# Kernel tuning notes

Measured on AMD Instinct MI355X. Metric: run time of the kernel, lower is better.

Reference implementation:

```python
import jax, jax.numpy as jnp
import numpy as np

C_CONST = 1.0
GAMMA = 1.0
GATE_EPS = 1e-9


def _gate(a, b):
    # smooth 'between' gate: ~1 when a*b < 0, ~0 when a*b > 0
    u = a * b
    return 0.5 * (1.0 - u / jnp.sqrt(u * u + GATE_EPS))


def _softmin2(a, b, gamma):
    return -gamma * jnp.logaddexp(-a / gamma, -b / gamma)


def _softmin3(a, b, c, gamma):
    s = jnp.stack([a, b, c], axis=0)
    return -gamma * jax.nn.logsumexp(-s / gamma, axis=0)


def _trans(x_val, y_prev, z_other, c, gamma):
    # MSM split/merge transition cost, soft version
    a = x_val - y_prev
    b = x_val - z_other
    g = _gate(a, b)
    return c + (1.0 - g) * _softmin2(a * a, b * b, gamma)


def _soft_msm_batched(xb, yb, c, gamma):
    # xb: (B, T), yb: (B, U) -> costs (B,)
    B, T = xb.shape
    U = yb.shape[1]
    # row 0: C[0,0] = (x0-y0)^2; C[0,j] = C[0,j-1] + trans(y_j, y_{j-1}, x_0)
    c00 = (xb[:, 0] - yb[:, 0]) ** 2                                  # (B,)
    left0 = _trans(yb[:, 1:], yb[:, :-1], xb[:, 0:1], c, gamma)       # (B, U-1)
    row0 = jnp.concatenate(
        [c00[:, None], c00[:, None] + jnp.cumsum(left0, axis=1)], axis=1
    )                                                                 # (B, U)

    def row_step(prev, xs):
        xi, xim1 = xs                                                 # (B,), (B,)
        match = (xi[:, None] - yb) ** 2                               # (B, U)
        up = _trans(xi[:, None], xim1[:, None], yb, c, gamma)         # (B, U)
        left = _trans(yb[:, 1:], yb[:, :-1], xi[:, None], c, gamma)   # (B, U-1)
        c_i0 = prev[:, 0] + up[:, 0]                                  # (B,)
        d_diag = prev[:, :-1] + match[:, 1:]                          # (B, U-1)
        d_up = prev[:, 1:] + up[:, 1:]                                # (B, U-1)

        def cell(c_left, z):
            dd, du, lf = z                                            # each (B,)
            cij = _softmin3(dd, du, c_left + lf, gamma)
            return cij, cij

        _, cells = jax.lax.scan(cell, c_i0, (d_diag.T, d_up.T, left.T))
        row = jnp.concatenate([c_i0[:, None], cells.T], axis=1)       # (B, U)
        return row, None

    last_row, _ = jax.lax.scan(row_step, row0, (xb[:, 1:].T, xb[:, :-1].T))
    return last_row[:, -1]                                            # (B,)


def setup_inputs() -> dict:
    key = jax.random.key(0)
    kx, ky = jax.random.split(key)
    x = jax.random.normal(kx, (64, 1, 512), dtype=jnp.float32)
    y = jax.random.normal(ky, (64, 1, 512), dtype=jnp.float32)
    return {"x": x, "y": y}


def reference(x, y):
    # SoftMSMLoss(c=1.0, gamma=1.0, reduction='mean', window=None)
    costs = _soft_msm_batched(x[:, 0, :], y[:, 0, :], C_CONST, GAMMA)
    return costs.mean()
```

## Files before the change

### kernel.cpp

```cpp
#include <hip/hip_runtime.h>
#include <math.h>
#include <type_traits>


#define TT 512
#define BATCH 64
#define G 8
#define NPH 128
#define C1F 1.2011224087864498f
#define C2F 2.8853900817779268f
#define K2F 0.13533528323661270f
#define LN2F 0.69314718055994531f
#define NEG_BIG (-1e30f)

#if __has_builtin(__builtin_amdgcn_exp2f)
#define EXP2F(x) __builtin_amdgcn_exp2f(x)
#else
#define EXP2F(x) __expf((x) * LN2F)
#endif

typedef float v2f __attribute__((ext_vector_type(2)));

__device__ __forceinline__ float dpp_shr1_f(float src, float old) {
  return __int_as_float(__builtin_amdgcn_update_dpp(
      __float_as_int(old), __float_as_int(src), 0x138, 0xF, 0xF, false));
}
__device__ __forceinline__ int dpp_shr1_i(int src, int old) {
  return __builtin_amdgcn_update_dpp(old, src, 0x138, 0xF, 0xF, false);
}

__global__ __launch_bounds__(128, 1) void msm_kernel(const float* __restrict__ x,
                                                     const float* __restrict__ y,
                                                     float* __restrict__ ws) {
  const int b = blockIdx.x;
  const int tid = threadIdx.x;
  const int wv = tid >> 6;
  const int j = tid & 63;
  const float* xb = x + b * TT;
  const float* yb = y + b * TT;

  __shared__ float2 FXC[NPH], FDX[NPH], FEX[NPH];
  __shared__ float2 BXA[NPH], BDX[NPH], BEX[NPH];
  __shared__ float LF[TT], LG[TT], TERMS[TT];

  if (wv == 0) {
    float4 xq = ((const float4*)xb)[j];
    float rx[4] = {xq.x, xq.y, xq.z, xq.w};
    float prev = (j > 0) ? xb[4 * j - 1] : 0.0f;
    float cc[4], dd[4], ee[4];
#pragma unroll
    for (int k = 0; k < 4; ++k) {
      float dx = rx[k] - prev;
      prev = rx[k];
      cc[k] = rx[k] * C1F;
      dd[k] = dx;
      ee[k] = __expf(-dx * dx);
    }
    FXC[2 * j] = make_float2(cc[0], cc[1]);
    FXC[2 * j + 1] = make_float2(cc[2], cc[3]);
    FDX[2 * j] = make_float2(dd[0], dd[1]);
    FDX[2 * j + 1] = make_float2(dd[2], dd[3]);
    FEX[2 * j] = make_float2(ee[0], ee[1]);
    FEX[2 * j + 1] = make_float2(ee[2], ee[3]);
  } else {
    float cc[4], dd[4], ee[4];
#pragma unroll
    for (int k = 0; k < 4; ++k) {
      int rp = 4 * j + k;
      int i1 = 512 - rp; if (i1 > 511) i1 = 511;
      int i2 = 511 - rp;
      float xa = xb[i1];
      float dxp = xb[i2] - xa;
      cc[k] = xa * C1F;
      dd[k] = dxp;
      ee[k] = __expf(-dxp * dxp);
    }
    BXA[2 * j] = make_float2(cc[0], cc[1]);
    BXA[2 * j + 1] = make_float2(cc[2], cc[3]);
    BDX[2 * j] = make_float2(dd[0], dd[1]);
    BDX[2 * j + 1] = make_float2(dd[2], dd[3]);
    BEX[2 * j] = make_float2(ee[0], ee[1]);
    BEX[2 * j + 1] = make_float2(ee[2], ee[3]);
  }
  __syncthreads();

  float EpF[G];
#pragma unroll
  for (int k = 0; k < G; ++k) EpF[k] = 0.0f;
  int kaccF = 0;

  if (wv == 0) {
    float yc[G], dyS[G], edy2[G];
    {
      const float4* yv = (const float4*)yb;
      float4 a0 = yv[j * 2], a1 = yv[j * 2 + 1];
      float ry[G] = {a0.x, a0.y, a0.z, a0.w, a1.x, a1.y, a1.z, a1.w};
      float prev = (j > 0) ? yb[8 * j - 1] : 0.0f;
#pragma unroll
      for (int k = 0; k < G; ++k) {
        float dy = ry[k] - prev;
        prev = ry[k];
        yc[k] = ry[k] * C1F;
        dyS[k] = dy;
        edy2[k] = __expf(-dy * dy);
      }
    }
    float dc0 = 0.0f, dc1 = 0.0f, dc2 = 0.0f;
    float2 rdEx = FXC[0], rdEd = FDX[0], rdEe = FEX[0];
    float2 rdOx, rdOd, rdOe;

    auto fstep = [&](int t, auto phc, float2& xcU, float2& dxU, float2& exU,
                     float2& xcL, float2& dxL, float2& exL) {
      constexpr int PH = decltype(phc)::value;
      {
        int pn = t + 2 - j;
        pn = (pn < 0) ? 0 : ((pn > NPH - 1) ? NPH - 1 : pn);
        xcL = FXC[pn]; dxL = FDX[pn]; exL = FEX[pn];
      }
      float r0 = dpp_shr1_f(dc0, 0.0f);
      float r1 = dpp_shr1_f(dc1, 0.0f);
      float r2 = dpp_shr1_f(dc2, 0.0f);
      int k_in = dpp_shr1_i(kaccF, kaccF);
      const int p = t - j;
      if (PH == 0) {
        if (t == 0 && j == 0) r0 = K2F;
      }
      bool act = true;
      int kacc_e = kaccF;
      if (PH == 0) { act = (p >= 0); kacc_e = (p == 0) ? k_in : kaccF; }
      else if (PH == 2) { act = (p < NPH); }
      const int knew = (k_in > kacc_e) ? k_in : kacc_e;
      const float mMe = ldexpf(1.0f, kacc_e - knew);
      const float mIn = ldexpf(1.0f, k_in - knew);
      const float dv0 = r0 * mIn, dv1 = r1 * mIn, dv2 = r2 * mIn;
      const float nd0 = dc2 * mMe;
      float u[G];
#pragma unroll
      for (int k = 0; k < G; ++k) u[k] = EpF[k] * mMe;

      const v2f xcp = {xcU.x, xcU.y};
      const v2f dxp = {dxU.x, dxU.y};
      const v2f exv = {exU.x, exU.y};
      v2f Aw[G], Bw[G], Cw[G];
#define WCELL(kk)                                                       \
      {                                                                 \
        v2f s1 = xcp - yc[kk];                                          \
        v2f arg = C2F - s1 * s1;                                        \
        v2f A;                                                          \
        A.x = EXP2F(arg.x);                                             \
        A.y = EXP2F(arg.y);                                             \
        v2f Bs = A * K2F + exv;                                         \
        v2f Cs = A * K2F + edy2[kk];                                    \
        v2f gu = dxp * s1;                                              \
        v2f gl = dyS[kk] * s1;                                          \
        Aw[kk] = A;                                                     \
        Bw[kk].x = (gu.x > 0.0f) ? Bs.x : 1.0f;                         \
        Bw[kk].y = (gu.y > 0.0f) ? Bs.y : 1.0f;                         \
        Cw[kk].x = (gl.x < 0.0f) ? Cs.x : 1.0f;                         \
        Cw[kk].y = (gl.y < 0.0f) ? Cs.y : 1.0f;                         \
      }
      WCELL(0) WCELL(1) WCELL(2)
      float T0[G], T1[G];
#pragma unroll
      for (int k = 0; k < G; ++k) {
        if (k + 3 < G) WCELL(k + 3)
        __builtin_amdgcn_sched_barrier(0);
        float da = (k == 0) ? dv0 : u[k - 1];
        float pa = __fmaf_rn(da, Aw[k].x, u[k] * Bw[k].x);
        T0[k] = __fmaf_rn((k == 0) ? dv1 : T0[k - 1], Cw[k].x, pa);
        float db = (k == 0) ? dv1 : T0[k - 1];
        float pb = __fmaf_rn(db, Aw[k].y, T0[k] * Bw[k].y);
        T1[k] = __fmaf_rn((k == 0) ? dv2 : T1[k - 1], Cw[k].y, pb);
      }
#undef WCELL
      const float ndc1 = T0[G - 1];
      float m0 = fmaxf(fmaxf(T1[0], T1[1]), T1[2]);
      float m1 = fmaxf(fmaxf(T1[3], T1[4]), T1[5]);
      float m2 = fmaxf(fmaxf(T1[6], T1[7]), nd0);
      float vmax = fmaxf(fmaxf(m0, m1), fmaxf(m2, ndc1));
      unsigned ue = (__float_as_uint(vmax) >> 23) & 0xFFu;
      int e = (int)ue - 126;
      float sc = ldexpf(1.0f, -e);
      if (PH == 1) {
#pragma unroll
        for (int k = 0; k < G; ++k) EpF[k] = T1[k] * sc;
        dc0 = nd0 * sc; dc1 = ndc1 * sc; dc2 = EpF[G - 1];
        kaccF = knew + e;
      } else {
#pragma unroll
        for (int k = 0; k < G; ++k) EpF[k] = act ? T1[k] * sc : EpF[k];
        dc0 = act ? nd0 * sc : dc0;
        dc1 = act ? ndc1 * sc : dc1;
        dc2 = act ? EpF[G - 1] : dc2;
        kaccF = act ? knew + e : kaccF;
      }
    };
    std::integral_constant<int, 0> P0;
    std::integral_constant<int, 1> P1;
    std::integral_constant<int, 2> P2;
    for (int t = 0; t < 64; t += 2) {
      fstep(t, P0, rdEx, rdEd, rdEe, rdOx, rdOd, rdOe);
      fstep(t + 1, P0, rdOx, rdOd, rdOe, rdEx, rdEd, rdEe);
    }
    for (int t = 64; t < 128; t += 2) {
      fstep(t, P1, rdEx, rdEd, rdEe, rdOx, rdOd, rdOe);
      fstep(t + 1, P1, rdOx, rdOd, rdOe, rdEx, rdEd, rdEe);
    }
    for (int t = 128; t < 192; t += 2) {
      fstep(t, P2, rdEx, rdEd, rdEe, rdOx, rdOd, rdOe);
      fstep(t + 1, P2, rdOx, rdOd, rdOe, rdEx, rdEd, rdEe);
    }
#pragma unroll
    for (int k = 0; k < G; ++k) {
      float le = (EpF[k] > 0.0f) ? __logf(EpF[k]) : NEG_BIG;
      LF[8 * j + k] = le + (float)kaccF * LN2F - (float)(255 + 8 * j + k);
    }
  } else {
    float ycP[G + 1], dyP[G], edy2P[G];
    {
#pragma unroll
      for (int k = 0; k <= G; ++k) {
        int idx = 512 - 8 * j - k; if (idx > 511) idx = 511;
        ycP[k] = yb[idx] * C1F;
      }
#pragma unroll
      for (int k = 0; k < G; ++k) {
        int ia = 511 - 8 * j - k;
        int ib = 512 - 8 * j - k; if (ib > 511) ib = 511;
        float d = yb[ia] - yb[ib];
        dyP[k] = d;
        edy2P[k] = __expf(-d * d);
      }
    }
    float dc0 = 0.0f, dc1 = 0.0f, dc2 = 0.0f;
    float sBk0[G + 1], eBk0[G + 1], sBk1[G + 1], eBk1[G + 1];
    {
      float xa0 = BXA[0].x;
#pragma unroll
      for (int k = 0; k <= G; ++k) {
        float s = xa0 - ycP[k];
        sBk0[k] = s;
        eBk0[k] = EXP2F(C2F - s * s);
      }
    }
    float2 cxA = BXA[0], cdx = BDX[0], cex = BEX[0];

    auto bstep = [&](int t, auto phc, float (&sU)[G + 1], float (&eU)[G + 1],
                     float (&sO)[G + 1], float (&eO)[G + 1]) {
      constexpr int PH = decltype(phc)::value;
      const int p = t - j;
      int pn = t + 1 - j;
      pn = (pn < 0) ? 0 : ((pn > NPH - 1) ? NPH - 1 : pn);
      float2 nxA = BXA[pn], ndx = BDX[pn], nex = BEX[pn];
      float r0 = dpp_shr1_f(dc0, 0.0f);
      float r1 = dpp_shr1_f(dc1, 0.0f);
      float r2 = dpp_shr1_f(dc2, 0.0f);
      int k_in = dpp_shr1_i(kaccF, kaccF);
      const bool seed = (PH == 0) && (t == 0) && (j == 0);
      if (seed) r0 = 1.0f;
      bool act = true;
      int kacc_e = kaccF;
      if (PH == 0) { act = (p >= 0); kacc_e = (p == 0) ? k_in : kaccF; }
      else if (PH == 2) { act = (p < NPH); }
      const int knew = (k_in > kacc_e) ? k_in : kacc_e;
      const float mMe = ldexpf(1.0f, kacc_e - knew);
      const float mIn = ldexpf(1.0f, k_in - knew);
      const float dv0 = r0 * mIn, dv1 = r1 * mIn, dv2 = r2 * mIn;
      const float nd0 = dc2 * mMe;
      float u[G];
#pragma unroll
      for (int k = 0; k < G; ++k) u[k] = EpF[k] * mMe;

      const v2f xbn = {cxA.y, nxA.x};
      float sV[G + 1], eV[G + 1];
#define BWIN(mm)                                                        \
      {                                                                 \
        v2f sw = xbn - ycP[mm];                                         \
        v2f arg = C2F - sw * sw;                                        \
        sV[mm] = sw.x;  eV[mm] = EXP2F(arg.x);                          \
        sO[mm] = sw.y;  eO[mm] = EXP2F(arg.y);                          \
      }
      BWIN(0) BWIN(1) BWIN(2) BWIN(3) BWIN(4)
      const float dxa = cdx.x, dxb = cdx.y, exa = cex.x, exb = cex.y;
      float T0[G], T1[G];
#pragma unroll
      for (int k = 0; k < G; ++k) {
        if (k + 5 <= G) BWIN(k + 5)
        __builtin_amdgcn_sched_barrier(0);
        float Aa = eU[k];
        if (seed && k == 0) Aa = 1.0f;
        float Ba = (dxa * sU[k + 1] < 0.0f) ? __fmaf_rn(eU[k + 1], K2F, exa) : 1.0f;
        float Ca = (dyP[k] * sV[k] > 0.0f) ? __fmaf_rn(eV[k], K2F, edy2P[k]) : 1.0f;
        float Ab = eV[k];
        float Bb = (dxb * sV[k + 1] < 0.0f) ? __fmaf_rn(eV[k + 1], K2F, exb) : 1.0f;
        float Cb = (dyP[k] * sO[k] > 0.0f) ? __fmaf_rn(eO[k], K2F, edy2P[k]) : 1.0f;
        float da = (k == 0) ? dv0 : u[k - 1];
        float pa = __fmaf_rn(da, Aa, u[k] * Ba);
        T0[k] = __fmaf_rn((k == 0) ? dv1 : T0[k - 1], Ca, pa);
        float db = (k == 0) ? dv1 : T0[k - 1];
        float pb = __fmaf_rn(db, Ab, T0[k] * Bb);
        T1[k] = __fmaf_rn((k == 0) ? dv2 : T1[k - 1], Cb, pb);
      }
#undef BWIN
      const float ndc1 = T0[G - 1];
      float m0 = fmaxf(fmaxf(T1[0], T1[1]), T1[2]);
      float m1 = fmaxf(fmaxf(T1[3], T1[4]), T1[5]);
      float m2 = fmaxf(fmaxf(T1[6], T1[7]), nd0);
      float vmax = fmaxf(fmaxf(m0, m1), fmaxf(m2, ndc1));
      unsigned ue = (__float_as_uint(vmax) >> 23) & 0xFFu;
      int e = (int)ue - 126;
      float sc = ldexpf(1.0f, -e);
      if (PH == 1) {
#pragma unroll
        for (int k = 0; k < G; ++k) EpF[k] = T1[k] * sc;
        dc0 = nd0 * sc; dc1 = ndc1 * sc; dc2 = EpF[G - 1];
        kaccF = knew + e;
      } else {
#pragma unroll
        for (int k = 0; k < G; ++k) EpF[k] = act ? T1[k] * sc : EpF[k];
        dc0 = act ? nd0 * sc : dc0;
        dc1 = act ? ndc1 * sc : dc1;
        dc2 = act ? EpF[G - 1] : dc2;
        kaccF = act ? knew + e : kaccF;
      }
      cxA = nxA; cdx = ndx; cex = nex;
    };
    std::integral_constant<int, 0> P0;
    std::integral_constant<int, 1> P1;
    std::integral_constant<int, 2> P2;
    for (int t = 0; t < 64; t += 2) {
      bstep(t, P0, sBk0, eBk0, sBk1, eBk1);
      bstep(t + 1, P0, sBk1, eBk1, sBk0, eBk0);
    }
    for (int t = 64; t < 128; t += 2) {
      bstep(t, P1, sBk0, eBk0, sBk1, eBk1);
      bstep(t + 1, P1, sBk1, eBk1, sBk0, eBk0);
    }
    for (int t = 128; t < 192; t += 2) {
      bstep(t, P2, sBk0, eBk0, sBk1, eBk1);
      bstep(t + 1, P2, sBk1, eBk1, sBk0, eBk0);
    }
#pragma unroll
    for (int k = 0; k < G; ++k) {
      float le = (EpF[k] > 0.0f) ? __logf(EpF[k]) : NEG_BIG;
      LG[511 - (8 * j + k)] = le + (float)kaccF * LN2F - (float)(255 + 8 * j + k);
    }
  }
  __syncthreads();

  {
    const float sx = xb[256];
    const float dxs = sx - xb[255];
    const float ex2s = __expf(-dxs * dxs);
#pragma unroll
    for (int c = 0; c < 4; ++c) {
      int jj = 4 * tid + c;
      float d = sx - yb[jj];
      float m2 = d * d;
      float lw = (dxs * d > 0.0f) ? __logf(ex2s + __expf(-m2)) : 0.0f;
      float t1 = ((jj > 0) ? LF[jj - 1] : NEG_BIG) - m2;
      float t2 = LF[jj] - 1.0f + lw;
      float mt = fmaxf(t1, t2);
      float term = NEG_BIG;
      if (mt > -1e29f)
        term = LG[jj] + mt + __logf(__expf(t1 - mt) + __expf(t2 - mt));
      TERMS[jj] = term;
    }
  }
  __syncthreads();
  if (wv == 0) {
    float v[8];
    float M = NEG_BIG;
#pragma unroll
    for (int i = 0; i < 8; ++i) {
      v[i] = TERMS[8 * j + i];
      M = fmaxf(M, v[i]);
    }
#pragma unroll
    for (int off = 1; off < 64; off <<= 1) M = fmaxf(M, __shfl_xor(M, off));
    float S = 0.0f;
#pragma unroll
    for (int i = 0; i < 8; ++i) S += __expf(v[i] - M);
#pragma unroll
    for (int off = 1; off < 64; off <<= 1) S += __shfl_xor(S, off);
    if (j == 0) ws[b] = -(M + __logf(S));
  }
}

__global__ __launch_bounds__(64) void reduce_kernel(const float* __restrict__ ws,
                                                    float* __restrict__ out) {
  float v = ws[threadIdx.x];
#pragma unroll
  for (int off = 32; off > 0; off >>= 1) v += __shfl_down(v, off);
  if (threadIdx.x == 0) out[0] = v * (1.0f / BATCH);
}

extern "C" void kernel_launch(void* const* d_in, const int* in_sizes, int n_in,
                              void* d_out, int out_size, void* d_ws, size_t ws_size,
                              hipStream_t stream) {
  const float* x = (const float*)d_in[0];
  const float* y = (const float*)d_in[1];
  float* ws = (float*)d_ws;
  float* out = (float*)d_out;
  msm_kernel<<<BATCH, 128, 0, stream>>>(x, y, ws);
  reduce_kernel<<<1, 64, 0, stream>>>(ws, out);
}
```

Before: 158.2 us.

## Pack four batch elements per workgroup with 512-thread blocks

Each workgroup now handles four batch elements (eight waves: a forward and a backward wave per element) instead of one element per 128-thread workgroup, and launches 16 blocks instead of 64. Shared-memory arrays gain a per-element index. The likely aim is to cut per-block launch and setup overhead and put several waves on the same CU. In exchange, only 16 CUs are used, so the four independent serial wavefront recurrences compete for the same SIMDs instead of each running on its own CU.

```diff
diff --git a/kernel.cpp b/kernel.cpp
--- a/kernel.cpp
+++ b/kernel.cpp
@@ -5,6 +5,7 @@
 
 #define TT 512
 #define BATCH 64
+#define BPB 4
 #define G 8
 #define NPH 128
 #define C1F 1.2011224087864498f
@@ -29,21 +30,23 @@
   return __builtin_amdgcn_update_dpp(old, src, 0x138, 0xF, 0xF, false);
 }
 
-__global__ __launch_bounds__(128, 1) void msm_kernel(const float* __restrict__ x,
+__global__ __launch_bounds__(512, 2) void msm_kernel(const float* __restrict__ x,
                                                      const float* __restrict__ y,
                                                      float* __restrict__ ws) {
-  const int b = blockIdx.x;
   const int tid = threadIdx.x;
-  const int wv = tid >> 6;
+  const int w = tid >> 6;
+  const int m = w >> 1;
+  const int dir = w & 1;
   const int j = tid & 63;
+  const int b = blockIdx.x * BPB + m;
   const float* xb = x + b * TT;
   const float* yb = y + b * TT;
 
-  __shared__ float2 FXC[NPH], FDX[NPH], FEX[NPH];
-  __shared__ float2 BXA[NPH], BDX[NPH], BEX[NPH];
-  __shared__ float LF[TT], LG[TT], TERMS[TT];
-
-  if (wv == 0) {
+  __shared__ float2 FXC[BPB][NPH], FDX[BPB][NPH], FEX[BPB][NPH];
+  __shared__ float2 BXA[BPB][NPH], BDX[BPB][NPH], BEX[BPB][NPH];
+  __shared__ float LF[BPB][TT], LG[BPB][TT], TERMS[BPB][TT];
+
+  if (dir == 0) {
     float4 xq = ((const float4*)xb)[j];
     float rx[4] = {xq.x, xq.y, xq.z, xq.w};
     float prev = (j > 0) ? xb[4 * j - 1] : 0.0f;
@@ -56,12 +59,12 @@
       dd[k] = dx;
       ee[k] = __expf(-dx * dx);
     }
-    FXC[2 * j] = make_float2(cc[0], cc[1]);
-    FXC[2 * j + 1] = make_float2(cc[2], cc[3]);
-    FDX[2 * j] = make_float2(dd[0], dd[1]);
-    FDX[2 * j + 1] = make_float2(dd[2], dd[3]);
-    FEX[2 * j] = make_float2(ee[0], ee[1]);
-    FEX[2 * j + 1] = make_float2(ee[2], ee[3]);
+    FXC[m][2 * j] = make_float2(cc[0], cc[1]);
+    FXC[m][2 * j + 1] = make_float2(cc[2], cc[3]);
+    FDX[m][2 * j] = make_float2(dd[0], dd[1]);
+    FDX[m][2 * j + 1] = make_float2(dd[2], dd[3]);
+    FEX[m][2 * j] = make_float2(ee[0], ee[1]);
+    FEX[m][2 * j + 1] = make_float2(ee[2], ee[3]);
   } else {
     float cc[4], dd[4], ee[4];
 #pragma unroll
@@ -75,12 +78,12 @@
       dd[k] = dxp;
       ee[k] = __expf(-dxp * dxp);
     }
-    BXA[2 * j] = make_float2(cc[0], cc[1]);
-    BXA[2 * j + 1] = make_float2(cc[2], cc[3]);
-    BDX[2 * j] = make_float2(dd[0], dd[1]);
-    BDX[2 * j + 1] = make_float2(dd[2], dd[3]);
-    BEX[2 * j] = make_float2(ee[0], ee[1]);
-    BEX[2 * j + 1] = make_float2(ee[2], ee[3]);
+    BXA[m][2 * j] = make_float2(cc[0], cc[1]);
+    BXA[m][2 * j + 1] = make_float2(cc[2], cc[3]);
+    BDX[m][2 * j] = make_float2(dd[0], dd[1]);
+    BDX[m][2 * j + 1] = make_float2(dd[2], dd[3]);
+    BEX[m][2 * j] = make_float2(ee[0], ee[1]);
+    BEX[m][2 * j + 1] = make_float2(ee[2], ee[3]);
   }
   __syncthreads();
 
@@ -89,7 +92,10 @@
   for (int k = 0; k < G; ++k) EpF[k] = 0.0f;
   int kaccF = 0;
 
-  if (wv == 0) {
+  if (dir == 0) {
+    const float2* __restrict__ pFXC = FXC[m];
+    const float2* __restrict__ pFDX = FDX[m];
+    const float2* __restrict__ pFEX = FEX[m];
     float yc[G], dyS[G], edy2[G];
     {
       const float4* yv = (const float4*)yb;
@@ -106,7 +112,7 @@
       }
     }
     float dc0 = 0.0f, dc1 = 0.0f, dc2 = 0.0f;
-    float2 rdEx = FXC[0], rdEd = FDX[0], rdEe = FEX[0];
+    float2 rdEx = pFXC[0], rdEd = pFDX[0], rdEe = pFEX[0];
     float2 rdOx, rdOd, rdOe;
 
     auto fstep = [&](int t, auto phc, float2& xcU, float2& dxU, float2& exU,
@@ -115,7 +121,7 @@
       {
         int pn = t + 2 - j;
         pn = (pn < 0) ? 0 : ((pn > NPH - 1) ? NPH - 1 : pn);
-        xcL = FXC[pn]; dxL = FDX[pn]; exL = FEX[pn];
+        xcL = pFXC[pn]; dxL = pFDX[pn]; exL = pFEX[pn];
       }
       float r0 = dpp_shr1_f(dc0, 0.0f);
       float r1 = dpp_shr1_f(dc1, 0.0f);
@@ -213,9 +219,12 @@
 #pragma unroll
     for (int k = 0; k < G; ++k) {
       float le = (EpF[k] > 0.0f) ? __logf(EpF[k]) : NEG_BIG;
-      LF[8 * j + k] = le + (float)kaccF * LN2F - (float)(255 + 8 * j + k);
+      LF[m][8 * j + k] = le + (float)kaccF * LN2F - (float)(255 + 8 * j + k);
     }
   } else {
+    const float2* __restrict__ pBXA = BXA[m];
+    const float2* __restrict__ pBDX = BDX[m];
+    const float2* __restrict__ pBEX = BEX[m];
     float ycP[G + 1], dyP[G], edy2P[G];
     {
 #pragma unroll
@@ -235,7 +244,7 @@
     float dc0 = 0.0f, dc1 = 0.0f, dc2 = 0.0f;
     float sBk0[G + 1], eBk0[G + 1], sBk1[G + 1], eBk1[G + 1];
     {
-      float xa0 = BXA[0].x;
+      float xa0 = pBXA[0].x;
 #pragma unroll
       for (int k = 0; k <= G; ++k) {
         float s = xa0 - ycP[k];
@@ -243,7 +252,7 @@
         eBk0[k] = EXP2F(C2F - s * s);
       }
     }
-    float2 cxA = BXA[0], cdx = BDX[0], cex = BEX[0];
+    float2 cxA = pBXA[0], cdx = pBDX[0], cex = pBEX[0];
 
     auto bstep = [&](int t, auto phc, float (&sU)[G + 1], float (&eU)[G + 1],
                      float (&sO)[G + 1], float (&eO)[G + 1]) {
@@ -251,7 +260,7 @@
       const int p = t - j;
       int pn = t + 1 - j;
       pn = (pn < 0) ? 0 : ((pn > NPH - 1) ? NPH - 1 : pn);
-      float2 nxA = BXA[pn], ndx = BDX[pn], nex = BEX[pn];
+      float2 nxA = pBXA[pn], ndx = pBDX[pn], nex = pBEX[pn];
       float r0 = dpp_shr1_f(dc0, 0.0f);
       float r1 = dpp_shr1_f(dc1, 0.0f);
       float r2 = dpp_shr1_f(dc2, 0.0f);
@@ -343,37 +352,38 @@
 #pragma unroll
     for (int k = 0; k < G; ++k) {
       float le = (EpF[k] > 0.0f) ? __logf(EpF[k]) : NEG_BIG;
-      LG[511 - (8 * j + k)] = le + (float)kaccF * LN2F - (float)(255 + 8 * j + k);
+      LG[m][511 - (8 * j + k)] = le + (float)kaccF * LN2F - (float)(255 + 8 * j + k);
     }
   }
   __syncthreads();
 
   {
+    const int gt = tid & 127;
     const float sx = xb[256];
     const float dxs = sx - xb[255];
     const float ex2s = __expf(-dxs * dxs);
 #pragma unroll
     for (int c = 0; c < 4; ++c) {
-      int jj = 4 * tid + c;
+      int jj = 4 * gt + c;
       float d = sx - yb[jj];
       float m2 = d * d;
       float lw = (dxs * d > 0.0f) ? __logf(ex2s + __expf(-m2)) : 0.0f;
-      float t1 = ((jj > 0) ? LF[jj - 1] : NEG_BIG) - m2;
-      float t2 = LF[jj] - 1.0f + lw;
+      float t1 = ((jj > 0) ? LF[m][jj - 1] : NEG_BIG) - m2;
+      float t2 = LF[m][jj] - 1.0f + lw;
       float mt = fmaxf(t1, t2);
       float term = NEG_BIG;
       if (mt > -1e29f)
-        term = LG[jj] + mt + __logf(__expf(t1 - mt) + __expf(t2 - mt));
-      TERMS[jj] = term;
+        term = LG[m][jj] + mt + __logf(__expf(t1 - mt) + __expf(t2 - mt));
+      TERMS[m][jj] = term;
     }
   }
   __syncthreads();
-  if (wv == 0) {
+  if (dir == 0) {
     float v[8];
     float M = NEG_BIG;
 #pragma unroll
     for (int i = 0; i < 8; ++i) {
-      v[i] = TERMS[8 * j + i];
+      v[i] = TERMS[m][8 * j + i];
       M = fmaxf(M, v[i]);
     }
 #pragma unroll
@@ -402,6 +412,6 @@
   const float* y = (const float*)d_in[1];
   float* ws = (float*)d_ws;
   float* out = (float*)d_out;
-  msm_kernel<<<BATCH, 128, 0, stream>>>(x, y, ws);
+  msm_kernel<<<BATCH / BPB, 512, 0, stream>>>(x, y, ws);
   reduce_kernel<<<1, 64, 0, stream>>>(ws, out);
 }
```

New measurement: 235.5 us. 1.49x slower.
